# Optimization experiments

Measured on AMD Instinct MI355X. Metric: run time of the kernel, lower is better.

The kernel has to match this reference:

```python
import jax, jax.numpy as jnp
import numpy as np

NB_LABELS = 8        # number of distinct node labels
NB_EDGE_LABELS = 4   # number of distinct edge (bond) labels
N = 32               # order of every graph (card_max, all graphs padded/equal)
SINKHORN_ITERS = 10  # svd.eps_assign2(..., 10)


def costs_from_weighs(node_weighs, edge_weighs):
    cn = jax.nn.relu(node_weighs)
    ce = jax.nn.relu(edge_weighs)
    iu = jnp.triu_indices(NB_LABELS, k=1)
    node_costs = jnp.zeros((NB_LABELS, NB_LABELS), dtype=cn.dtype).at[iu].set(cn[:-1])
    node_costs = node_costs + node_costs.T
    iu2 = jnp.triu_indices(NB_EDGE_LABELS, k=1)
    edge_costs = jnp.zeros((NB_EDGE_LABELS, NB_EDGE_LABELS), dtype=ce.dtype).at[iu2].set(ce[:-1])
    edge_costs = edge_costs + edge_costs.T
    return node_costs, cn[-1], edge_costs, ce[-1]


def sinkhorn(S, iters):
    # eps-assignment: alternate row/col normalization, last row/col scale fixed to 1
    for _ in range(iters):
        r = 1.0 / S.sum(axis=1)
        r = r.at[-1].set(1.0)
        S = S * r[:, None]
        c = 1.0 / S.sum(axis=0)
        c = c.at[-1].set(1.0)
        S = S * c[None, :]
    return S


def pair_ged(A1, A2, l1, l2, node_costs, nodeInsDel, edge_costs, edgeInsDel):
    # A1, A2: (N+1, N+1) int padded labeled adjacency; l1, l2: (N,) int node labels
    n1 = N + 1
    b1 = A1 != 0
    b2 = A2 != 0
    # edge insertion/deletion indicator: (not e1 and e2) or (e1 and not e2)
    ins_del = jnp.logical_or(
        jnp.einsum('ij,kl->ijkl', ~b1, b2),
        jnp.einsum('ij,kl->ijkl', b1, ~b2)).astype(jnp.float32)
    # edge substitution: sum_{p!=q} edge_costs[p,q] * [A1==p+1] * [A2==q+1]
    lab_ids = jnp.arange(1, NB_EDGE_LABELS + 1)
    E1 = (A1[None] == lab_ids[:, None, None]).astype(jnp.float32)  # (L, n1, n1)
    E2 = (A2[None] == lab_ids[:, None, None]).astype(jnp.float32)
    subst = jnp.einsum('pij,qkl,pq->ijkl', E1, E2, edge_costs)  # diag(edge_costs)=0
    C4 = edgeInsDel * ins_del + subst
    # torch cat/unbind reshuffle: C[(j,k),(i,l)] = C4[i,j,k,l]
    C = jnp.transpose(C4, (1, 2, 0, 3)).reshape(n1 * n1, n1 * n1)
    # diagonal vector D: node subst for (i<N, j<N), nodeInsDel on last row/col, 0 at corner
    Dmat = jnp.full((n1, n1), nodeInsDel, dtype=jnp.float32)
    Dmat = Dmat.at[:N, :N].set(node_costs[l1][:, l2])
    Dmat = Dmat.at[N, N].set(0.0)
    c_diag = Dmat.reshape(-1)                       # diag(C) after masking
    Doff = C * (1.0 - jnp.eye(n1 * n1, dtype=C.dtype))  # C with diagonal zeroed
    # mapping_from_cost returns x0 = sinkhorn(exp(-0.5*c), 10)
    v = sinkhorn(jnp.exp(-0.5 * Dmat), SINKHORN_ITERS).reshape(-1)
    return 0.5 * (v @ (Doff @ v)) + c_diag @ v


def setup_inputs() -> dict:
    key = jax.random.key(0)
    k1, k2, k3, k4, k5 = jax.random.split(key, 5)
    G, P = 64, 64
    nw = 0.01 * (1.0 + 0.1 * jax.random.uniform(k1, (NB_LABELS * (NB_LABELS - 1) // 2 + 1,)))
    nw = nw.at[-1].set(0.03)
    ew = 0.01 * (1.0 + 0.1 * jax.random.uniform(k2, (NB_EDGE_LABELS * (NB_EDGE_LABELS - 1) // 2 + 1,)))
    ew = ew.at[-1].set(0.02)
    R = jax.random.randint(k3, (G, N, N), 0, NB_EDGE_LABELS + 1)
    Au = jnp.triu(R, 1)
    A = (Au + jnp.transpose(Au, (0, 2, 1))).astype(jnp.int32)  # symmetric labeled adjacency
    labels = jax.random.randint(k4, (G, N), 0, NB_LABELS, dtype=jnp.int32)
    pairs = jax.random.randint(k5, (P, 2), 0, G, dtype=jnp.int32)
    return {"node_weighs": nw.astype(jnp.float32), "edge_weighs": ew.astype(jnp.float32),
            "A": A, "labels": labels, "pairs": pairs}


def reference(node_weighs, edge_weighs, A, labels, pairs):
    node_costs, nodeInsDel, edge_costs, edgeInsDel = costs_from_weighs(node_weighs, edge_weighs)
    A1 = jnp.pad(A[pairs[:, 0]], ((0, 0), (0, 1), (0, 1)))  # (P, N+1, N+1)
    A2 = jnp.pad(A[pairs[:, 1]], ((0, 0), (0, 1), (0, 1)))
    l1 = labels[pairs[:, 0]]
    l2 = labels[pairs[:, 1]]
    ged = jax.vmap(pair_ged, in_axes=(0, 0, 0, 0, None, None, None, None))(
        A1, A2, l1, l2, node_costs, nodeInsDel, edge_costs, edgeInsDel)
    return (ged - ged.min()) / (ged.max() - ged.min())
```

## Files before the change

kernel.cpp:

```cpp
#include <hip/hip_runtime.h>
#include <math.h>
#include <stdint.h>

constexpr int NQ    = 33;
constexpr int NQP   = 34;
constexpr int NSQ   = NQ * NQ;
constexpr int NL    = 8;
constexpr int NEL   = 4;
constexpr int NN    = 32;
constexpr int ITERS = 10;
constexpr int BLK   = 1024;

__global__ __launch_bounds__(BLK, 1) void ged_kernel(
    const float* __restrict__ nw, const float* __restrict__ ew,
    const int* __restrict__ A, const int* __restrict__ labels,
    const int* __restrict__ pairs, float* __restrict__ ged_ws)
{
    __shared__ float S[NQ][NQP];
    __shared__ float S0T[NQ][NQP];
    __shared__ float H[5][NQ][NQP];
    __shared__ unsigned char A1s[NQ][36];
    __shared__ unsigned char A2s[NQ][36];
    __shared__ float ncost[NL][NL];
    __shared__ float encost[NL][NL];
    __shared__ float ec[NEL][NEL];
    __shared__ float rr[NQ], cc[NQ];
    __shared__ float sNID, sEID, sENID;
    __shared__ int l1s[NN], l2s[NN];
    __shared__ float wredq[BLK/64], wredl[BLK/64];

    const int t  = threadIdx.x;
    const int p  = blockIdx.x;
    const int g1 = pairs[2*p+0], g2 = pairs[2*p+1];

    if (t < 28) {
        int i = (t>=27)?6 : (t>=25)?5 : (t>=22)?4 : (t>=18)?3 : (t>=13)?2 : (t>=7)?1 : 0;
        int off = (i==0)?0 : (i==1)?7 : (i==2)?13 : (i==3)?18 : (i==4)?22 : (i==5)?25 : 27;
        int j = t - off + i + 1;
        float v = fmaxf(nw[t], 0.f);
        ncost[i][j] = v; ncost[j][i] = v;
        float e = __expf(-0.5f * v);
        encost[i][j] = e; encost[j][i] = e;
    } else if (t == 28) {
        float v = fmaxf(nw[28], 0.f);
        sNID = v; sENID = __expf(-0.5f * v);
    } else if (t >= 32 && t < 38) {
        int q = t - 32;
        int ei = (q<3)?0 : (q<5)?1 : 2;
        int ej = (q<3)?q+1 : (q<5)?q-1 : 3;
        float v = fmaxf(ew[q], 0.f);
        ec[ei][ej] = v; ec[ej][ei] = v;
    } else if (t == 38) {
        sEID = fmaxf(ew[6], 0.f);
    } else if (t >= 40 && t < 48) {
        int q = t - 40;
        ncost[q][q] = 0.f; encost[q][q] = 1.f;
    } else if (t >= 48 && t < 52) {
        int q = t - 48;
        ec[q][q] = 0.f;
    } else if (t >= 56 && t < 56 + NQ) {
        cc[t - 56] = 1.f;
    }
    if (t >= 64  && t < 64 + NN)  l1s[t - 64]  = labels[g1*NN + (t - 64)];
    if (t >= 96  && t < 96 + NN)  l2s[t - 96]  = labels[g2*NN + (t - 96)];
    for (int c0 = t; c0 < NSQ; c0 += BLK) {
        int i = c0 / NQ, j = c0 - i*NQ;
        int a1 = (i < NN && j < NN) ? A[g1*NN*NN + i*NN + j] : 0;
        int a2 = (i < NN && j < NN) ? A[g2*NN*NN + i*NN + j] : 0;
        A1s[i][j] = (unsigned char)a1;
        A2s[i][j] = (unsigned char)a2;
    }
    __syncthreads();

    const float NID = sNID, EID = sEID, ENID = sENID;

    for (int c0 = t; c0 < NSQ; c0 += BLK) {
        int i = c0 / NQ, j = c0 - i*NQ;
        float e = (i < NN && j < NN) ? encost[l1s[i]][l2s[j]]
                                     : ((i == NN && j == NN) ? 1.f : ENID);
        S[i][j]   = e;
        S0T[j][i] = e;
    }
    __syncthreads();

    if (t < NQ) {
        for (int it = 0; it < ITERS; ++it) {
            float s = 0.f;
            #pragma unroll
            for (int j = 0; j < NQ; ++j) s += S[t][j] * cc[j];
            rr[t] = (t == NQ-1) ? 1.f : __builtin_amdgcn_rcpf(s);
            float s2 = 0.f;
            #pragma unroll
            for (int i2 = 0; i2 < NQ; ++i2) s2 += S0T[t][i2] * rr[i2];
            cc[t] = (t == NQ-1) ? 1.f : __builtin_amdgcn_rcpf(s2);
        }
    }
    __syncthreads();

    for (int c0 = t; c0 < NSQ; c0 += BLK) {
        int i = c0 / NQ, j = c0 - i*NQ;
        S[i][j] *= rr[i] * cc[j];
    }
    __syncthreads();

    for (int c0 = t; c0 < NSQ; c0 += BLK) {
        int i = c0 / NQ, k = c0 - i*NQ;
        const float* Si = &S[i][0];
        const uint32_t* Aw = (const uint32_t*)&A2s[k][0];
        float p0=0.f, p1=0.f, p2=0.f, p3=0.f, p4=0.f;
        #pragma unroll
        for (int l = 0; l < NQ; ++l) {
            float v = Si[l];
            int a2 = (int)((Aw[l >> 2] >> ((l & 3) * 8)) & 255u);
            p0 += (a2 == 0) ? v : 0.f;
            p1 += (a2 == 1) ? v : 0.f;
            p2 += (a2 == 2) ? v : 0.f;
            p3 += (a2 == 3) ? v : 0.f;
            p4 += (a2 == 4) ? v : 0.f;
        }
        H[0][i][k] = EID * (p1 + p2 + p3 + p4);
        #pragma unroll
        for (int x = 1; x <= 4; ++x) {
            H[x][i][k] = EID * p0
                       + ec[x-1][0]*p1 + ec[x-1][1]*p2
                       + ec[x-1][2]*p3 + ec[x-1][3]*p4;
        }
    }
    __syncthreads();

    float qpart = 0.f, lpart = 0.f;
    const float* Hb = &H[0][0][0];
    for (int c0 = t; c0 < NSQ; c0 += BLK) {
        int i = c0 / NQ, j = c0 - i*NQ;
        int x = A1s[i][j];
        const float* Hx = Hb + x*(NQ*NQP) + i*NQP;
        const float* Sj = &S[j][0];
        float dot = 0.f;
        #pragma unroll
        for (int k = 0; k < NQ; ++k) dot += Sj[k] * Hx[k];
        qpart += dot;
        float d = (i < NN && j < NN) ? ncost[l1s[i]][l2s[j]]
                                     : ((i == NN && j == NN) ? 0.f : NID);
        lpart += d * S[i][j];
    }

    #pragma unroll
    for (int off = 32; off > 0; off >>= 1) {
        qpart += __shfl_down(qpart, off);
        lpart += __shfl_down(lpart, off);
    }
    if ((t & 63) == 0) { wredq[t>>6] = qpart; wredl[t>>6] = lpart; }
    __syncthreads();
    if (t == 0) {
        float q = 0.f, l = 0.f;
        #pragma unroll
        for (int w = 0; w < BLK/64; ++w) { q += wredq[w]; l += wredl[w]; }
        ged_ws[p] = 0.5f * q + l;
    }
}

__global__ __launch_bounds__(64) void norm_kernel(
    const float* __restrict__ ged, float* __restrict__ out, int P)
{
    int t = threadIdx.x;
    float mn = 1e30f, mx = -1e30f;
    for (int i = t; i < P; i += 64) {
        float g = ged[i];
        mn = fminf(mn, g); mx = fmaxf(mx, g);
    }
    #pragma unroll
    for (int off = 32; off > 0; off >>= 1) {
        mn = fminf(mn, __shfl_xor(mn, off));
        mx = fmaxf(mx, __shfl_xor(mx, off));
    }
    float inv = 1.f / (mx - mn);
    for (int i = t; i < P; i += 64) out[i] = (ged[i] - mn) * inv;
}

extern "C" void kernel_launch(void* const* d_in, const int* in_sizes, int n_in,
                              void* d_out, int out_size, void* d_ws, size_t ws_size,
                              hipStream_t stream) {
    const float* nw     = (const float*)d_in[0];
    const float* ew     = (const float*)d_in[1];
    const int*   A      = (const int*)d_in[2];
    const int*   labels = (const int*)d_in[3];
    const int*   pairs  = (const int*)d_in[4];
    const int P = in_sizes[4] / 2;

    float* ged_ws = (float*)d_ws;

    ged_kernel<<<P, BLK, 0, stream>>>(nw, ew, A, labels, pairs, ged_ws);
    norm_kernel<<<1, 64, 0, stream>>>(ged_ws, (float*)d_out, P);
}
```

Measured before the change: 20.97 us.

## Run Sinkhorn in registers on one wave, overlapped with LDS setup

The Sinkhorn row/column normalisation moves out of shared memory into a single wavefront. Each lane holds half a row and half a column of the similarity matrix in registers and exchanges scale factors with ds_bpermute and shfl_xor. Meanwhile the other 15 waves load the adjacency tiles and build S, so the setup barrier, the separate cost-table initialisation and the transposed copy S0T go away. Edge and node costs are computed directly from the weights instead of from shared tables. In exchange, the label lookups and exp evaluations are repeated more often and register pressure in wave 0 rises.

```diff
diff --git a/kernel.cpp b/kernel.cpp
--- a/kernel.cpp
+++ b/kernel.cpp
@@ -5,11 +5,15 @@
 constexpr int NQ    = 33;
 constexpr int NQP   = 34;
 constexpr int NSQ   = NQ * NQ;
-constexpr int NL    = 8;
-constexpr int NEL   = 4;
 constexpr int NN    = 32;
 constexpr int ITERS = 10;
 constexpr int BLK   = 1024;
+
+__device__ __forceinline__ float node_cost(int a, int b, const float* __restrict__ nw) {
+    if (a == b) return 0.f;
+    int lo = min(a, b), hi = max(a, b);
+    return fmaxf(nw[lo * (15 - lo) / 2 + hi - lo - 1], 0.f);
+}
 
 __global__ __launch_bounds__(BLK, 1) void ged_kernel(
     const float* __restrict__ nw, const float* __restrict__ ew,
@@ -17,82 +21,91 @@
     const int* __restrict__ pairs, float* __restrict__ ged_ws)
 {
     __shared__ float S[NQ][NQP];
-    __shared__ float S0T[NQ][NQP];
     __shared__ float H[5][NQ][NQP];
     __shared__ unsigned char A1s[NQ][36];
     __shared__ unsigned char A2s[NQ][36];
-    __shared__ float ncost[NL][NL];
-    __shared__ float encost[NL][NL];
-    __shared__ float ec[NEL][NEL];
+    __shared__ float ncost_s[8][8];
     __shared__ float rr[NQ], cc[NQ];
-    __shared__ float sNID, sEID, sENID;
-    __shared__ int l1s[NN], l2s[NN];
     __shared__ float wredq[BLK/64], wredl[BLK/64];
 
     const int t  = threadIdx.x;
     const int p  = blockIdx.x;
     const int g1 = pairs[2*p+0], g2 = pairs[2*p+1];
 
-    if (t < 28) {
-        int i = (t>=27)?6 : (t>=25)?5 : (t>=22)?4 : (t>=18)?3 : (t>=13)?2 : (t>=7)?1 : 0;
-        int off = (i==0)?0 : (i==1)?7 : (i==2)?13 : (i==3)?18 : (i==4)?22 : (i==5)?25 : 27;
-        int j = t - off + i + 1;
-        float v = fmaxf(nw[t], 0.f);
-        ncost[i][j] = v; ncost[j][i] = v;
-        float e = __expf(-0.5f * v);
-        encost[i][j] = e; encost[j][i] = e;
-    } else if (t == 28) {
-        float v = fmaxf(nw[28], 0.f);
-        sNID = v; sENID = __expf(-0.5f * v);
-    } else if (t >= 32 && t < 38) {
-        int q = t - 32;
-        int ei = (q<3)?0 : (q<5)?1 : 2;
-        int ej = (q<3)?q+1 : (q<5)?q-1 : 3;
-        float v = fmaxf(ew[q], 0.f);
-        ec[ei][ej] = v; ec[ej][ei] = v;
-    } else if (t == 38) {
-        sEID = fmaxf(ew[6], 0.f);
-    } else if (t >= 40 && t < 48) {
-        int q = t - 40;
-        ncost[q][q] = 0.f; encost[q][q] = 1.f;
-    } else if (t >= 48 && t < 52) {
-        int q = t - 48;
-        ec[q][q] = 0.f;
-    } else if (t >= 56 && t < 56 + NQ) {
-        cc[t - 56] = 1.f;
-    }
-    if (t >= 64  && t < 64 + NN)  l1s[t - 64]  = labels[g1*NN + (t - 64)];
-    if (t >= 96  && t < 96 + NN)  l2s[t - 96]  = labels[g2*NN + (t - 96)];
-    for (int c0 = t; c0 < NSQ; c0 += BLK) {
-        int i = c0 / NQ, j = c0 - i*NQ;
-        int a1 = (i < NN && j < NN) ? A[g1*NN*NN + i*NN + j] : 0;
-        int a2 = (i < NN && j < NN) ? A[g2*NN*NN + i*NN + j] : 0;
-        A1s[i][j] = (unsigned char)a1;
-        A2s[i][j] = (unsigned char)a2;
-    }
-    __syncthreads();
-
-    const float NID = sNID, EID = sEID, ENID = sENID;
-
-    for (int c0 = t; c0 < NSQ; c0 += BLK) {
-        int i = c0 / NQ, j = c0 - i*NQ;
-        float e = (i < NN && j < NN) ? encost[l1s[i]][l2s[j]]
-                                     : ((i == NN && j == NN) ? 1.f : ENID);
-        S[i][j]   = e;
-        S0T[j][i] = e;
-    }
-    __syncthreads();
-
-    if (t < NQ) {
+    const float e01 = fmaxf(ew[0], 0.f), e02 = fmaxf(ew[1], 0.f), e03 = fmaxf(ew[2], 0.f);
+    const float e12 = fmaxf(ew[3], 0.f), e13 = fmaxf(ew[4], 0.f), e23 = fmaxf(ew[5], 0.f);
+    const float EID = fmaxf(ew[6], 0.f);
+    const float NID = fmaxf(nw[28], 0.f);
+    const float ENID = __expf(-0.5f * NID);
+
+    const int wid = t >> 6;
+    if (wid == 0) {
+        const int lane = t;
+        const int half = lane >> 5;
+        const int id   = lane & 31;
+        const int l1_self = labels[g1*NN + id];
+        const int l2_self = labels[g2*NN + id];
+
+        float sreg[17], treg[17];
+        int   idxr[17];
+        #pragma unroll
+        for (int m = 0; m < 17; ++m) {
+            int hs = 17 + m;
+            int src = half ? ((hs <= 31) ? hs : 63) : m;
+            idxr[m] = src << 2;
+        }
+        #pragma unroll
+        for (int m = 0; m < 15; ++m) {
+            int j = half * 17 + m;
+            sreg[m] = __expf(-0.5f * node_cost(l1_self, labels[g2*NN + j], nw));
+            treg[m] = __expf(-0.5f * node_cost(labels[g1*NN + j], l2_self, nw));
+        }
+        if (!half) {
+            sreg[15] = __expf(-0.5f * node_cost(l1_self, labels[g2*NN + 15], nw));
+            treg[15] = __expf(-0.5f * node_cost(labels[g1*NN + 15], l2_self, nw));
+            sreg[16] = __expf(-0.5f * node_cost(l1_self, labels[g2*NN + 16], nw));
+            treg[16] = __expf(-0.5f * node_cost(labels[g1*NN + 16], l2_self, nw));
+        } else {
+            sreg[15] = ENID; treg[15] = ENID;
+            sreg[16] = 0.f;  treg[16] = 0.f;
+        }
+
+        float cval = 1.0f, rval;
         for (int it = 0; it < ITERS; ++it) {
-            float s = 0.f;
+            float part = 0.f;
             #pragma unroll
-            for (int j = 0; j < NQ; ++j) s += S[t][j] * cc[j];
-            rr[t] = (t == NQ-1) ? 1.f : __builtin_amdgcn_rcpf(s);
-            float s2 = 0.f;
+            for (int m = 0; m < 17; ++m)
+                part += sreg[m] * __int_as_float(
+                    __builtin_amdgcn_ds_bpermute(idxr[m], __float_as_int(cval)));
+            part += __shfl_xor(part, 32);
+            rval = __builtin_amdgcn_rcpf(part);
+            if (lane == 63) rval = 1.0f;
+            float part2 = 0.f;
             #pragma unroll
-            for (int i2 = 0; i2 < NQ; ++i2) s2 += S0T[t][i2] * rr[i2];
-            cc[t] = (t == NQ-1) ? 1.f : __builtin_amdgcn_rcpf(s2);
+            for (int m = 0; m < 17; ++m)
+                part2 += treg[m] * __int_as_float(
+                    __builtin_amdgcn_ds_bpermute(idxr[m], __float_as_int(rval)));
+            part2 += __shfl_xor(part2, 32);
+            cval = __builtin_amdgcn_rcpf(part2);
+            if (lane == 63) cval = 1.0f;
+        }
+        if (!half) { rr[id] = rval; cc[id] = cval; }
+        if (lane == 32) { rr[32] = 1.f; cc[32] = 1.f; }
+    } else {
+        const int t2 = t - 64;
+        if (t2 < 64) ncost_s[t2 >> 3][t2 & 7] = node_cost(t2 >> 3, t2 & 7, nw);
+        for (int c0 = t2; c0 < NSQ; c0 += BLK - 64) {
+            int i = c0 / NQ, j = c0 - i*NQ;
+            int a1 = (i < NN && j < NN) ? A[g1*NN*NN + i*NN + j] : 0;
+            int a2 = (i < NN && j < NN) ? A[g2*NN*NN + i*NN + j] : 0;
+            A1s[i][j] = (unsigned char)a1;
+            A2s[i][j] = (unsigned char)a2;
+            float e;
+            if (i < NN && j < NN)
+                e = __expf(-0.5f * node_cost(labels[g1*NN + i], labels[g2*NN + j], nw));
+            else
+                e = (i == NN && j == NN) ? 1.f : ENID;
+            S[i][j] = e;
         }
     }
     __syncthreads();
@@ -119,12 +132,10 @@
             p4 += (a2 == 4) ? v : 0.f;
         }
         H[0][i][k] = EID * (p1 + p2 + p3 + p4);
-        #pragma unroll
-        for (int x = 1; x <= 4; ++x) {
-            H[x][i][k] = EID * p0
-                       + ec[x-1][0]*p1 + ec[x-1][1]*p2
-                       + ec[x-1][2]*p3 + ec[x-1][3]*p4;
-        }
+        H[1][i][k] = EID * p0 +            e01*p2 + e02*p3 + e03*p4;
+        H[2][i][k] = EID * p0 + e01*p1 +            e12*p3 + e13*p4;
+        H[3][i][k] = EID * p0 + e02*p1 + e12*p2 +            e23*p4;
+        H[4][i][k] = EID * p0 + e03*p1 + e13*p2 + e23*p3;
     }
     __syncthreads();
 
@@ -139,8 +150,9 @@
         #pragma unroll
         for (int k = 0; k < NQ; ++k) dot += Sj[k] * Hx[k];
         qpart += dot;
-        float d = (i < NN && j < NN) ? ncost[l1s[i]][l2s[j]]
-                                     : ((i == NN && j == NN) ? 0.f : NID);
+        float d;
+        if (i < NN && j < NN) d = ncost_s[labels[g1*NN + i]][labels[g2*NN + j]];
+        else                  d = (i == NN && j == NN) ? 0.f : NID;
         lpart += d * S[i][j];
     }
 
```

Measured after the change: 24.79 us. 18.2% more time.

## Register-tile final contraction, derive p0 from row sums, split Sinkhorn accumulators

Applied to the files above, without the earlier changes.

The final quadratic contraction now uses 363 threads, each holding one S column row in registers and reusing it across three i rows, instead of every thread reloading S[j] for one element. The H build drops the p0 accumulator and takes it as the Sinkhorn row sum minus the labeled partials; that row sum is computed once after the iterations. The Sinkhorn dot products use four independent accumulators, and the last reduction uses shuffles. This cuts LDS traffic and serial dependency chains, but most threads sit idle in the contraction and register pressure goes up.

```diff
diff --git a/kernel.cpp b/kernel.cpp
--- a/kernel.cpp
+++ b/kernel.cpp
@@ -4,6 +4,7 @@
 
 constexpr int NQ    = 33;
 constexpr int NQP   = 34;
+constexpr int HP    = 36;
 constexpr int NSQ   = NQ * NQ;
 constexpr int NL    = 8;
 constexpr int NEL   = 4;
@@ -16,18 +17,18 @@
     const int* __restrict__ A, const int* __restrict__ labels,
     const int* __restrict__ pairs, float* __restrict__ ged_ws)
 {
-    __shared__ float S[NQ][NQP];
-    __shared__ float S0T[NQ][NQP];
-    __shared__ float H[5][NQ][NQP];
+    __shared__ __align__(16) float S[NQ][NQP];
+    __shared__ __align__(16) float S0T[NQ][NQP];
+    __shared__ __align__(16) float H[5][NQ][HP];
     __shared__ unsigned char A1s[NQ][36];
     __shared__ unsigned char A2s[NQ][36];
     __shared__ float ncost[NL][NL];
     __shared__ float encost[NL][NL];
     __shared__ float ec[NEL][NEL];
-    __shared__ float rr[NQ], cc[NQ];
+    __shared__ __align__(16) float rr[NQ], cc[NQ], rsum[NQ];
     __shared__ float sNID, sEID, sENID;
     __shared__ int l1s[NN], l2s[NN];
-    __shared__ float wredq[BLK/64], wredl[BLK/64];
+    __shared__ float wredq[16], wredl[16];
 
     const int t  = threadIdx.x;
     const int p  = blockIdx.x;
@@ -73,6 +74,8 @@
     __syncthreads();
 
     const float NID = sNID, EID = sEID, ENID = sENID;
+    const float e01 = ec[0][1], e02 = ec[0][2], e03 = ec[0][3];
+    const float e12 = ec[1][2], e13 = ec[1][3], e23 = ec[2][3];
 
     for (int c0 = t; c0 < NSQ; c0 += BLK) {
         int i = c0 / NQ, j = c0 - i*NQ;
@@ -84,16 +87,36 @@
     __syncthreads();
 
     if (t < NQ) {
+        const float* Srow = &S[t][0];
+        const float* Trow = &S0T[t][0];
+        float rval = 1.f;
         for (int it = 0; it < ITERS; ++it) {
-            float s = 0.f;
+            float a0=0.f, a1=0.f, a2=0.f, a3=0.f;
             #pragma unroll
-            for (int j = 0; j < NQ; ++j) s += S[t][j] * cc[j];
-            rr[t] = (t == NQ-1) ? 1.f : __builtin_amdgcn_rcpf(s);
-            float s2 = 0.f;
+            for (int j = 0; j < 32; j += 4) {
+                a0 += Srow[j+0]*cc[j+0]; a1 += Srow[j+1]*cc[j+1];
+                a2 += Srow[j+2]*cc[j+2]; a3 += Srow[j+3]*cc[j+3];
+            }
+            float s = ((a0+a1)+(a2+a3)) + Srow[32]*cc[32];
+            rval = (t == NQ-1) ? 1.f : __builtin_amdgcn_rcpf(s);
+            rr[t] = rval;
+            float b0=0.f, b1=0.f, b2=0.f, b3=0.f;
             #pragma unroll
-            for (int i2 = 0; i2 < NQ; ++i2) s2 += S0T[t][i2] * rr[i2];
+            for (int j = 0; j < 32; j += 4) {
+                b0 += Trow[j+0]*rr[j+0]; b1 += Trow[j+1]*rr[j+1];
+                b2 += Trow[j+2]*rr[j+2]; b3 += Trow[j+3]*rr[j+3];
+            }
+            float s2 = ((b0+b1)+(b2+b3)) + Trow[32]*rr[32];
             cc[t] = (t == NQ-1) ? 1.f : __builtin_amdgcn_rcpf(s2);
         }
+        float a0=0.f, a1=0.f, a2=0.f, a3=0.f;
+        #pragma unroll
+        for (int j = 0; j < 32; j += 4) {
+            a0 += Srow[j+0]*cc[j+0]; a1 += Srow[j+1]*cc[j+1];
+            a2 += Srow[j+2]*cc[j+2]; a3 += Srow[j+3]*cc[j+3];
+        }
+        float sf = ((a0+a1)+(a2+a3)) + Srow[32]*cc[32];
+        rsum[t] = rval * sf;
     }
     __syncthreads();
 
@@ -107,41 +130,54 @@
         int i = c0 / NQ, k = c0 - i*NQ;
         const float* Si = &S[i][0];
         const uint32_t* Aw = (const uint32_t*)&A2s[k][0];
-        float p0=0.f, p1=0.f, p2=0.f, p3=0.f, p4=0.f;
+        float p1=0.f, p2=0.f, p3=0.f, p4=0.f;
         #pragma unroll
         for (int l = 0; l < NQ; ++l) {
             float v = Si[l];
-            int a2 = (int)((Aw[l >> 2] >> ((l & 3) * 8)) & 255u);
-            p0 += (a2 == 0) ? v : 0.f;
-            p1 += (a2 == 1) ? v : 0.f;
-            p2 += (a2 == 2) ? v : 0.f;
-            p3 += (a2 == 3) ? v : 0.f;
-            p4 += (a2 == 4) ? v : 0.f;
-        }
-        H[0][i][k] = EID * (p1 + p2 + p3 + p4);
-        #pragma unroll
-        for (int x = 1; x <= 4; ++x) {
-            H[x][i][k] = EID * p0
-                       + ec[x-1][0]*p1 + ec[x-1][1]*p2
-                       + ec[x-1][2]*p3 + ec[x-1][3]*p4;
-        }
+            int a2v = (int)((Aw[l >> 2] >> ((l & 3) * 8)) & 255u);
+            p1 += (a2v == 1) ? v : 0.f;
+            p2 += (a2v == 2) ? v : 0.f;
+            p3 += (a2v == 3) ? v : 0.f;
+            p4 += (a2v == 4) ? v : 0.f;
+        }
+        float t4 = (p1 + p2) + (p3 + p4);
+        float p0 = rsum[i] - t4;
+        H[0][i][k] = EID * t4;
+        H[1][i][k] = EID * p0 +            e01*p2 + e02*p3 + e03*p4;
+        H[2][i][k] = EID * p0 + e01*p1 +            e12*p3 + e13*p4;
+        H[3][i][k] = EID * p0 + e02*p1 + e12*p2 +            e23*p4;
+        H[4][i][k] = EID * p0 + e03*p1 + e13*p2 + e23*p3;
     }
     __syncthreads();
 
     float qpart = 0.f, lpart = 0.f;
-    const float* Hb = &H[0][0][0];
-    for (int c0 = t; c0 < NSQ; c0 += BLK) {
-        int i = c0 / NQ, j = c0 - i*NQ;
-        int x = A1s[i][j];
-        const float* Hx = Hb + x*(NQ*NQP) + i*NQP;
-        const float* Sj = &S[j][0];
-        float dot = 0.f;
-        #pragma unroll
-        for (int k = 0; k < NQ; ++k) dot += Sj[k] * Hx[k];
-        qpart += dot;
-        float d = (i < NN && j < NN) ? ncost[l1s[i]][l2s[j]]
-                                     : ((i == NN && j == NN) ? 0.f : NID);
-        lpart += d * S[i][j];
+    if (t < 363) {
+        const int j  = t / 11;
+        const int ig = t - j*11;
+        float Vr[34];
+        const float2* Sj2 = (const float2*)&S[j][0];
+        #pragma unroll
+        for (int m = 0; m < 17; ++m) {
+            float2 w = Sj2[m];
+            Vr[2*m] = w.x; Vr[2*m+1] = w.y;
+        }
+        #pragma unroll
+        for (int ii = 0; ii < 3; ++ii) {
+            const int i = ig*3 + ii;
+            const int x = A1s[i][j];
+            const float* Hx = &H[x][i][0];
+            float d0=0.f, d1=0.f, d2=0.f, d3=0.f;
+            #pragma unroll
+            for (int k = 0; k < 32; k += 4) {
+                d0 += Vr[k+0]*Hx[k+0]; d1 += Vr[k+1]*Hx[k+1];
+                d2 += Vr[k+2]*Hx[k+2]; d3 += Vr[k+3]*Hx[k+3];
+            }
+            qpart += ((d0+d1)+(d2+d3)) + Vr[32]*Hx[32];
+            float d;
+            if (i < NN && j < NN) d = ncost[l1s[i]][l2s[j]];
+            else                  d = (i == NN && j == NN) ? 0.f : NID;
+            lpart += d * S[i][j];
+        }
     }
 
     #pragma unroll
@@ -151,11 +187,13 @@
     }
     if ((t & 63) == 0) { wredq[t>>6] = qpart; wredl[t>>6] = lpart; }
     __syncthreads();
-    if (t == 0) {
-        float q = 0.f, l = 0.f;
-        #pragma unroll
-        for (int w = 0; w < BLK/64; ++w) { q += wredq[w]; l += wredl[w]; }
-        ged_ws[p] = 0.5f * q + l;
+    if (t < 16) {
+        float q = wredq[t], l = wredl[t];
+        q += __shfl_down(q, 8); l += __shfl_down(l, 8);
+        q += __shfl_down(q, 4); l += __shfl_down(l, 4);
+        q += __shfl_down(q, 2); l += __shfl_down(l, 2);
+        q += __shfl_down(q, 1); l += __shfl_down(l, 1);
+        if (t == 0) ged_ws[p] = 0.5f * q + l;
     }
 }
 
```

Measured after the change: 21.13 us. Within noise of the previous version (+0.8%).
